# Kernel optimization log

Measured on AMD Instinct MI355X. Metric: run time of the kernel, lower is better.

## Reference

```python
import jax, jax.numpy as jnp
import numpy as np
import math

HEAD = 4
D_MODEL = 128
N_NODES = 2048
SEQ_LEN = 1
D_K = D_MODEL // HEAD
BATCH = 64


def conv1x1_relu(x, w, b):
    # x: [B, C, N, L], w: [O, C], b: [O]  (1x1 Conv2d + ReLU; dropout is identity in eval)
    return jax.nn.relu(jnp.einsum('oc,bcnl->bonl', w, x) + b[None, :, None, None])


def setup_inputs() -> dict:
    key = jax.random.key(0)
    ks = jax.random.split(key, 12)
    s = 0.05
    return {
        'x': jax.random.normal(ks[0], (BATCH, D_MODEL, N_NODES, SEQ_LEN), jnp.float32),
        'q_w': jax.random.normal(ks[1], (D_MODEL, D_MODEL), jnp.float32) * s,
        'q_b': jnp.zeros((D_MODEL,), jnp.float32),
        'v_w': jax.random.normal(ks[2], (D_MODEL, D_MODEL), jnp.float32) * s,
        'v_b': jnp.zeros((D_MODEL,), jnp.float32),
        'c_w': jax.random.normal(ks[3], (D_MODEL, D_MODEL), jnp.float32) * s,
        'c_b': jnp.zeros((D_MODEL,), jnp.float32),
        'memory': jax.random.normal(ks[4], (HEAD, SEQ_LEN, N_NODES, D_K), jnp.float32) * s,
        'nodevec1': jax.random.normal(ks[5], (N_NODES, 10), jnp.float32),
        'nodevec2': jax.random.normal(ks[6], (10, N_NODES), jnp.float32),
        'weights_pool': jax.random.normal(ks[7], (SEQ_LEN, 3, 3), jnp.float32) * s,
        'bias_pool': jax.random.normal(ks[8], (N_NODES, D_K), jnp.float32) * s,
        'aff_w': jnp.ones((D_MODEL, N_NODES, SEQ_LEN), jnp.float32),
        'aff_b': jnp.zeros((D_MODEL, N_NODES, SEQ_LEN), jnp.float32),
    }


def reference(x, q_w, q_b, v_w, v_b, c_w, c_b, memory, nodevec1, nodevec2,
              weights_pool, bias_pool, aff_w, aff_b):
    B = x.shape[0]
    scale = math.sqrt(D_K)

    query = conv1x1_relu(x, q_w, q_b)
    value = conv1x1_relu(x, v_w, v_b)

    # [B, d_model, N, L] -> [B, h, d_k, N, L] -> [B, h, L, N, d_k]
    def split_heads(t):
        return t.reshape(B, HEAD, D_K, N_NODES, SEQ_LEN).transpose(0, 1, 4, 3, 2)

    query = split_heads(query)
    value = split_heads(value)

    key_ = jax.nn.softmax(memory / scale, axis=-1)      # [h, L, N, d_k]
    query = jax.nn.softmax(query / scale, axis=-1)      # [B, h, L, N, d_k]

    Aapt = jax.nn.softmax(jax.nn.relu(nodevec1 @ nodevec2), axis=-1)  # [N, N]

    kv = jnp.einsum('hlnx,bhlny->bhlxy', key_, value)          # [B,h,L,d_k,d_k]
    attn_qkv = jnp.einsum('bhlnx,bhlxy->bhlny', query, kv)     # [B,h,L,N,d_k]

    weights = jnp.einsum('nm,dio->nio', Aapt, weights_pool)    # [N,3,3]
    bias_dyn = Aapt @ bias_pool                                # [N,d_k]
    attn_dyn = jnp.einsum('bhlnc,nio->bhlnc', value, weights) + bias_dyn[None, None, None, :, :]

    out = attn_qkv + attn_dyn                                  # [B,h,L,N,d_k]
    out = out.transpose(0, 1, 4, 3, 2).reshape(B, D_MODEL, N_NODES, SEQ_LEN)
    out = conv1x1_relu(out, c_w, c_b)

    # num_nodes (2048) not in [170, 358, 5] -> affine-residual branch runs
    out = out * aff_w[None] + aff_b[None] + out
    return out
```

## Files before the change

kernel.cpp:

```cpp
#include <hip/hip_runtime.h>

#define NB 64
#define CH 128
#define NNODE 2048
#define NH 4
#define DKK 32
#define INVS 0.17677669529663687f

typedef __bf16 bf16x8 __attribute__((ext_vector_type(8)));
typedef float f32x4 __attribute__((ext_vector_type(4)));
typedef unsigned short ushort_t;

union U16x8 { uint4 u; bf16x8 b; unsigned short s[8]; };

__device__ inline bf16x8 as_bf16x8(uint4 u){ U16x8 x; x.u = u; return x.b; }
__device__ inline unsigned short f2b(float f){ __bf16 h = (__bf16)f; return __builtin_bit_cast(unsigned short, h); }
__device__ inline float b2f(unsigned short u){ __bf16 h = __builtin_bit_cast(__bf16, u); return (float)h; }

__global__ __launch_bounds__(256) void k0_prep(const float* __restrict__ qw,
    const float* __restrict__ vw, const float* __restrict__ cw,
    const float* __restrict__ memory, const float* __restrict__ bias_pool,
    ushort_t* __restrict__ wqb, ushort_t* __restrict__ wvb, ushort_t* __restrict__ wcb,
    ushort_t* __restrict__ keysT, float* __restrict__ bias_dyn,
    ushort_t* __restrict__ bpT)
{
  int gid = blockIdx.x * 256 + threadIdx.x;
  if (gid < 16384) { wqb[gid] = f2b(qw[gid]); wvb[gid] = f2b(vw[gid]); wcb[gid] = f2b(cw[gid]); }
  bias_dyn[gid] = 0.f;
  { int k = gid >> 11, m = gid & 2047;
    bpT[gid] = f2b(bias_pool[m * 32 + k]); }
  if (gid < 8192) {
    int h = gid >> 11, n = gid & 2047;
    const float* src = memory + (size_t)gid * 32;
    float v[32]; float m = -1e30f;
    #pragma unroll
    for (int i = 0; i < 32; ++i) { v[i] = src[i] * INVS; m = fmaxf(m, v[i]); }
    float s = 0.f;
    #pragma unroll
    for (int i = 0; i < 32; ++i) { v[i] = __expf(v[i] - m); s += v[i]; }
    float inv = 1.f / s;
    #pragma unroll
    for (int i = 0; i < 32; ++i)
      keysT[(size_t)(h * 32 + i) * 2048 + n] = f2b(v[i] * inv);
  }
}

__global__ __launch_bounds__(256) void kb1(const float* __restrict__ nv1,
    const float* __restrict__ nv2, ushort_t* __restrict__ Ebuf)
{
  int n = blockIdx.x; int tid = threadIdx.x;
  float a1[10];
  #pragma unroll
  for (int d = 0; d < 10; ++d) a1[d] = nv1[n * 10 + d];
  int m0 = tid * 8;
  float s[8];
  #pragma unroll
  for (int j = 0; j < 8; ++j) s[j] = 0.f;
  #pragma unroll
  for (int d = 0; d < 10; ++d) {
    const float* p = nv2 + d * 2048 + m0;
    float4 u = *(const float4*)p; float4 v = *(const float4*)(p + 4);
    s[0] += a1[d] * u.x; s[1] += a1[d] * u.y; s[2] += a1[d] * u.z; s[3] += a1[d] * u.w;
    s[4] += a1[d] * v.x; s[5] += a1[d] * v.y; s[6] += a1[d] * v.z; s[7] += a1[d] * v.w;
  }
  float e[8]; float sum = 0.f;
  #pragma unroll
  for (int j = 0; j < 8; ++j) { e[j] = __expf(fmaxf(s[j], 0.f)); sum += e[j]; }
  #pragma unroll
  for (int d = 1; d < 64; d <<= 1) sum += __shfl_xor(sum, d);
  __shared__ float red[4];
  if ((tid & 63) == 0) red[tid >> 6] = sum;
  __syncthreads();
  float inv = 1.f / (red[0] + red[1] + red[2] + red[3]);
  U16x8 o;
  #pragma unroll
  for (int j = 0; j < 8; ++j) o.s[j] = f2b(e[j] * inv);
  *(uint4*)(Ebuf + (size_t)n * 2048 + m0) = o.u;
}

__global__ __launch_bounds__(256) void kb2(const ushort_t* __restrict__ Ebuf,
    const ushort_t* __restrict__ bpT, float* __restrict__ bias_dyn)
{
  int bid = blockIdx.x;
  int n0 = (bid >> 3) * 128;
  int m0 = (bid & 7) * 256;
  int tid = threadIdx.x; int wv = tid >> 6; int lane = tid & 63;
  int quad = lane >> 4; int l16 = lane & 15;
  int r0 = n0 + 32 * wv;
  f32x4 zero4 = {0.f,0.f,0.f,0.f};
  f32x4 acc[2][2];
  acc[0][0] = zero4; acc[0][1] = zero4; acc[1][0] = zero4; acc[1][1] = zero4;
  for (int ks = 0; ks < 256; ks += 32) {
    int mb = m0 + ks + 8 * quad;
    bf16x8 a0 = *(const bf16x8*)(Ebuf + (size_t)(r0 + l16) * 2048 + mb);
    bf16x8 a1 = *(const bf16x8*)(Ebuf + (size_t)(r0 + 16 + l16) * 2048 + mb);
    bf16x8 b0 = *(const bf16x8*)(bpT + (size_t)l16 * 2048 + mb);
    bf16x8 b1 = *(const bf16x8*)(bpT + (size_t)(16 + l16) * 2048 + mb);
    acc[0][0] = __builtin_amdgcn_mfma_f32_16x16x32_bf16(a0, b0, acc[0][0], 0, 0, 0);
    acc[0][1] = __builtin_amdgcn_mfma_f32_16x16x32_bf16(a0, b1, acc[0][1], 0, 0, 0);
    acc[1][0] = __builtin_amdgcn_mfma_f32_16x16x32_bf16(a1, b0, acc[1][0], 0, 0, 0);
    acc[1][1] = __builtin_amdgcn_mfma_f32_16x16x32_bf16(a1, b1, acc[1][1], 0, 0, 0);
  }
  #pragma unroll
  for (int rt = 0; rt < 2; ++rt)
    #pragma unroll
    for (int ct = 0; ct < 2; ++ct)
      #pragma unroll
      for (int r = 0; r < 4; ++r)
        atomicAdd(bias_dyn + (size_t)(r0 + 16*rt + 4*quad + r) * 32 + 16*ct + l16,
                  acc[rt][ct][r]);
}

__global__ __launch_bounds__(256) void k1_qv(const float* __restrict__ x,
    const ushort_t* __restrict__ wqb, const ushort_t* __restrict__ wvb,
    const float* __restrict__ qbias, const float* __restrict__ vbias,
    ushort_t* __restrict__ QsT, ushort_t* __restrict__ VT)
{
  int bid = blockIdx.x; int b = bid >> 6; int n0 = (bid & 63) * 32;
  int tid = threadIdx.x; int wv = tid >> 6; int lane = tid & 63;
  int quad = lane >> 4; int l16 = lane & 15;
  __shared__ __align__(16) ushort_t XT[32][136];

  uint4 wq[2][4], wvv[2][4];
  #pragma unroll
  for (int ct = 0; ct < 2; ++ct)
    #pragma unroll
    for (int k0 = 0; k0 < 4; ++k0) {
      int off = (32 * wv + 16 * ct + l16) * 128 + 32 * k0 + 8 * quad;
      wq[ct][k0]  = *(const uint4*)(wqb + off);
      wvv[ct][k0] = *(const uint4*)(wvb + off);
    }
  float qb[2], vb[2];
  #pragma unroll
  for (int ct = 0; ct < 2; ++ct) {
    qb[ct] = qbias[32 * wv + 16 * ct + l16];
    vb[ct] = vbias[32 * wv + 16 * ct + l16];
  }

  #pragma unroll
  for (int p = 0; p < 4; ++p) {
    int c = 32 * p + (tid >> 3); int i = tid & 7;
    float4 v4 = *(const float4*)(x + (size_t)(b * 128 + c) * 2048 + n0 + 4 * i);
    XT[4*i+0][c] = f2b(v4.x); XT[4*i+1][c] = f2b(v4.y);
    XT[4*i+2][c] = f2b(v4.z); XT[4*i+3][c] = f2b(v4.w);
  }
  __syncthreads();

  f32x4 zero4 = {0.f,0.f,0.f,0.f};
  f32x4 accq[2][2], accv[2][2];
  #pragma unroll
  for (int i = 0; i < 2; ++i)
    #pragma unroll
    for (int j = 0; j < 2; ++j) { accq[i][j] = zero4; accv[i][j] = zero4; }

  #pragma unroll
  for (int k0 = 0; k0 < 4; ++k0) {
    bf16x8 a0 = *(const bf16x8*)&XT[l16][32 * k0 + 8 * quad];
    bf16x8 a1 = *(const bf16x8*)&XT[16 + l16][32 * k0 + 8 * quad];
    #pragma unroll
    for (int ct = 0; ct < 2; ++ct) {
      accq[0][ct] = __builtin_amdgcn_mfma_f32_16x16x32_bf16(a0, as_bf16x8(wq[ct][k0]),  accq[0][ct], 0, 0, 0);
      accq[1][ct] = __builtin_amdgcn_mfma_f32_16x16x32_bf16(a1, as_bf16x8(wq[ct][k0]),  accq[1][ct], 0, 0, 0);
      accv[0][ct] = __builtin_amdgcn_mfma_f32_16x16x32_bf16(a0, as_bf16x8(wvv[ct][k0]), accv[0][ct], 0, 0, 0);
      accv[1][ct] = __builtin_amdgcn_mfma_f32_16x16x32_bf16(a1, as_bf16x8(wvv[ct][k0]), accv[1][ct], 0, 0, 0);
    }
  }

  #pragma unroll
  for (int nt = 0; nt < 2; ++nt) {
    float sq[2][4];
    #pragma unroll
    for (int ct = 0; ct < 2; ++ct)
      #pragma unroll
      for (int r = 0; r < 4; ++r)
        sq[ct][r] = fmaxf(accq[nt][ct][r] + qb[ct], 0.f) * INVS;
    #pragma unroll
    for (int r = 0; r < 4; ++r) {
      float m = fmaxf(sq[0][r], sq[1][r]);
      m = fmaxf(m, __shfl_xor(m, 1)); m = fmaxf(m, __shfl_xor(m, 2));
      m = fmaxf(m, __shfl_xor(m, 4)); m = fmaxf(m, __shfl_xor(m, 8));
      float e0 = __expf(sq[0][r] - m), e1 = __expf(sq[1][r] - m);
      float s = e0 + e1;
      s += __shfl_xor(s, 1); s += __shfl_xor(s, 2);
      s += __shfl_xor(s, 4); s += __shfl_xor(s, 8);
      float inv = 1.f / s;
      accq[nt][0][r] = e0 * inv; accq[nt][1][r] = e1 * inv;
    }
    #pragma unroll
    for (int ct = 0; ct < 2; ++ct)
      #pragma unroll
      for (int r = 0; r < 4; ++r)
        accv[nt][ct][r] = fmaxf(accv[nt][ct][r] + vb[ct], 0.f);
  }

  __syncthreads();
  #pragma unroll
  for (int nt = 0; nt < 2; ++nt)
    #pragma unroll
    for (int ct = 0; ct < 2; ++ct)
      #pragma unroll
      for (int r = 0; r < 4; ++r)
        XT[16*nt + 4*quad + r][32*wv + 16*ct + l16] = f2b(accq[nt][ct][r]);
  __syncthreads();
  #pragma unroll
  for (int j = 0; j < 2; ++j) {
    int id = tid + 256 * j; int n = id >> 4; int u = id & 15;
    *(uint4*)(QsT + (size_t)(b * 2048 + n0 + n) * 128 + 8 * u) = *(uint4*)&XT[n][8 * u];
  }
  __syncthreads();
  #pragma unroll
  for (int nt = 0; nt < 2; ++nt)
    #pragma unroll
    for (int ct = 0; ct < 2; ++ct)
      #pragma unroll
      for (int r = 0; r < 4; ++r)
        XT[16*nt + 4*quad + r][32*wv + 16*ct + l16] = f2b(accv[nt][ct][r]);
  __syncthreads();
  #pragma unroll
  for (int j = 0; j < 2; ++j) {
    int id = tid + 256 * j; int n = id >> 4; int u = id & 15;
    *(uint4*)(VT + (size_t)(b * 2048 + n0 + n) * 128 + 8 * u) = *(uint4*)&XT[n][8 * u];
  }
}

__global__ __launch_bounds__(256) void k2_kv(const ushort_t* __restrict__ keysT,
    const ushort_t* __restrict__ VT, float* __restrict__ kvp)
{
  int bid = blockIdx.x; int b = bid >> 3; int nb = (bid & 7) * 256;
  int tid = threadIdx.x; int wv = tid >> 6; int lane = tid & 63;
  int quad = lane >> 4; int l16 = lane & 15;
  __shared__ __align__(16) ushort_t Vraw[128][136];

  f32x4 zero4 = {0.f,0.f,0.f,0.f};
  f32x4 acc[2][2];
  acc[0][0] = zero4; acc[0][1] = zero4; acc[1][0] = zero4; acc[1][1] = zero4;

  for (int chunk = 0; chunk < 2; ++chunk) {
    int nc = nb + 128 * chunk;
    if (chunk) __syncthreads();
    #pragma unroll
    for (int p = 0; p < 8; ++p) {
      int id = tid + 256 * p; int n = id >> 4; int g = id & 15;
      *(uint4*)&Vraw[n][8 * g] = *(const uint4*)(VT + (size_t)(b * 2048 + nc + n) * 128 + 8 * g);
    }
    __syncthreads();
    const ushort_t* kT = keysT + (size_t)(wv * 32) * 2048 + nc;
    #pragma unroll
    for (int ks = 0; ks < 4; ++ks) {
      int k0 = 32 * ks + 8 * quad;
      bf16x8 a0 = *(const bf16x8*)(kT + (size_t)l16 * 2048 + k0);
      bf16x8 a1 = *(const bf16x8*)(kT + (size_t)(16 + l16) * 2048 + k0);
      U16x8 b0, b1;
      #pragma unroll
      for (int j = 0; j < 8; ++j) {
        b0.s[j] = Vraw[k0 + j][32 * wv + l16];
        b1.s[j] = Vraw[k0 + j][32 * wv + 16 + l16];
      }
      acc[0][0] = __builtin_amdgcn_mfma_f32_16x16x32_bf16(a0, b0.b, acc[0][0], 0, 0, 0);
      acc[0][1] = __builtin_amdgcn_mfma_f32_16x16x32_bf16(a0, b1.b, acc[0][1], 0, 0, 0);
      acc[1][0] = __builtin_amdgcn_mfma_f32_16x16x32_bf16(a1, b0.b, acc[1][0], 0, 0, 0);
      acc[1][1] = __builtin_amdgcn_mfma_f32_16x16x32_bf16(a1, b1.b, acc[1][1], 0, 0, 0);
    }
  }

  float* dst = kvp + (size_t)bid * 4096 + wv * 1024;
  #pragma unroll
  for (int yt = 0; yt < 2; ++yt)
    #pragma unroll
    for (int xt = 0; xt < 2; ++xt)
      #pragma unroll
      for (int r = 0; r < 4; ++r)
        dst[(16 * yt + l16) * 32 + 16 * xt + 4 * quad + r] = acc[xt][yt][r];
}

__global__ __launch_bounds__(256) void kred(const float* __restrict__ kvp,
    float* __restrict__ kvws)
{
  int gid = blockIdx.x * 256 + threadIdx.x;
  int b = gid >> 12; int i = gid & 4095;
  const float* p = kvp + (size_t)(b * 8) * 4096 + i;
  float s = 0.f;
  #pragma unroll
  for (int t = 0; t < 8; ++t) s += p[t * 4096];
  kvws[gid] = s;
}

__global__ __launch_bounds__(256) void k3_out(const ushort_t* __restrict__ QsT,
    const ushort_t* __restrict__ VT, const float* __restrict__ kvws,
    const float* __restrict__ bias_dyn, const ushort_t* __restrict__ wcb,
    const float* __restrict__ cbias, const float* __restrict__ wpool,
    const float* __restrict__ aff_w, const float* __restrict__ aff_b,
    float* __restrict__ out)
{
  int bid = blockIdx.x; int b = bid >> 5; int n0 = (bid & 31) * 64;
  int tid = threadIdx.x; int wv = tid >> 6; int lane = tid & 63;
  int quad = lane >> 4; int l16 = lane & 15;
  __shared__ __align__(16) ushort_t kvT[4][32][40];
  __shared__ __align__(16) ushort_t MID[64][136];
  __shared__ __align__(16) ushort_t VL[64][132];
  __shared__ __align__(16) float    BD[64][36];

  float Ws = 0.f;
  #pragma unroll
  for (int i = 0; i < 9; ++i) Ws += wpool[i];

  uint4 wc[2][4];
  #pragma unroll
  for (int mt = 0; mt < 2; ++mt)
    #pragma unroll
    for (int k0 = 0; k0 < 4; ++k0)
      wc[mt][k0] = *(const uint4*)(wcb + (32 * wv + 16 * mt + l16) * 128 + 32 * k0 + 8 * quad);

  #pragma unroll
  for (int p = 0; p < 16; ++p) {
    int id = tid + 256 * p;
    kvT[id >> 10][(id >> 5) & 31][id & 31] = f2b(kvws[(size_t)b * 4096 + id]);
  }
  #pragma unroll
  for (int p = 0; p < 4; ++p) {
    int id = tid + 256 * p; int n = id >> 4; int u = id & 15;
    *(uint4*)&VL[n][8 * u] = *(const uint4*)(VT + (size_t)(b * 2048 + n0 + n) * 128 + 8 * u);
  }
  #pragma unroll
  for (int p = 0; p < 2; ++p) {
    int id = tid + 256 * p; int n = id >> 3; int g = id & 7;
    *(float4*)&BD[n][4 * g] = *(const float4*)(bias_dyn + (size_t)(n0 + n) * 32 + 4 * g);
  }
  __syncthreads();

  f32x4 zero4 = {0.f,0.f,0.f,0.f};
  f32x4 acc1[4][2];
  #pragma unroll
  for (int nt = 0; nt < 4; ++nt) { acc1[nt][0] = zero4; acc1[nt][1] = zero4; }
  #pragma unroll
  for (int nt = 0; nt < 4; ++nt) {
    bf16x8 aq = *(const bf16x8*)(QsT + (size_t)(b * 2048 + n0 + 16 * nt + l16) * 128 + 32 * wv + 8 * quad);
    #pragma unroll
    for (int ct = 0; ct < 2; ++ct)
      acc1[nt][ct] = __builtin_amdgcn_mfma_f32_16x16x32_bf16(
          aq, *(const bf16x8*)&kvT[wv][16 * ct + l16][8 * quad], acc1[nt][ct], 0, 0, 0);
  }

  #pragma unroll
  for (int nt = 0; nt < 4; ++nt)
    #pragma unroll
    for (int ct = 0; ct < 2; ++ct)
      #pragma unroll
      for (int r = 0; r < 4; ++r) {
        int nl = 16 * nt + 4 * quad + r;
        int cc = 32 * wv + 16 * ct + l16;
        float v = b2f(VL[nl][cc]);
        float bd = BD[nl][16 * ct + l16];
        MID[nl][cc] = f2b(acc1[nt][ct][r] + Ws * v + bd);
      }
  __syncthreads();

  f32x4 acc2[2][4];
  #pragma unroll
  for (int mt = 0; mt < 2; ++mt)
    #pragma unroll
    for (int nt = 0; nt < 4; ++nt) acc2[mt][nt] = zero4;
  #pragma unroll
  for (int k0 = 0; k0 < 4; ++k0) {
    bf16x8 bb[4];
    #pragma unroll
    for (int nt = 0; nt < 4; ++nt)
      bb[nt] = *(const bf16x8*)&MID[16 * nt + l16][32 * k0 + 8 * quad];
    #pragma unroll
    for (int mt = 0; mt < 2; ++mt)
      #pragma unroll
      for (int nt = 0; nt < 4; ++nt)
        acc2[mt][nt] = __builtin_amdgcn_mfma_f32_16x16x32_bf16(
            as_bf16x8(wc[mt][k0]), bb[nt], acc2[mt][nt], 0, 0, 0);
  }

  #pragma unroll
  for (int mt = 0; mt < 2; ++mt)
    #pragma unroll
    for (int nt = 0; nt < 4; ++nt)
      #pragma unroll
      for (int r = 0; r < 4; ++r) {
        int c_out = 32 * wv + 16 * mt + 4 * quad + r;
        int nn2 = n0 + 16 * nt + l16;
        float yv = fmaxf(acc2[mt][nt][r] + cbias[c_out], 0.f);
        size_t ai = (size_t)c_out * 2048 + nn2;
        float awv = aff_w[ai], abv = aff_b[ai];
        out[(size_t)(b * 128 + c_out) * 2048 + nn2] = yv * awv + abv + yv;
      }
}

extern "C" void kernel_launch(void* const* d_in, const int* in_sizes, int n_in,
                              void* d_out, int out_size, void* d_ws, size_t ws_size,
                              hipStream_t stream)
{
  const float* x      = (const float*)d_in[0];
  const float* qw     = (const float*)d_in[1];
  const float* qb     = (const float*)d_in[2];
  const float* vw     = (const float*)d_in[3];
  const float* vb     = (const float*)d_in[4];
  const float* cw     = (const float*)d_in[5];
  const float* cb     = (const float*)d_in[6];
  const float* memory = (const float*)d_in[7];
  const float* nv1    = (const float*)d_in[8];
  const float* nv2    = (const float*)d_in[9];
  const float* wpool  = (const float*)d_in[10];
  const float* bpool  = (const float*)d_in[11];
  const float* aw     = (const float*)d_in[12];
  const float* ab     = (const float*)d_in[13];
  float* out = (float*)d_out;

  char* ws = (char*)d_ws;
  ushort_t* QsT      = (ushort_t*)(ws);
  ushort_t* VT       = (ushort_t*)(ws + 33554432);
  float*    kvws     = (float*)   (ws + 67108864);
  ushort_t* keysT    = (ushort_t*)(ws + 68157440);
  float*    bias_dyn = (float*)   (ws + 69206016);
  ushort_t* wqb      = (ushort_t*)(ws + 69468160);
  ushort_t* wvb      = (ushort_t*)(ws + 69500928);
  ushort_t* wcb      = (ushort_t*)(ws + 69533696);
  ushort_t* Ebuf     = (ushort_t*)(ws + 69566464);
  ushort_t* bpT      = (ushort_t*)(ws + 77955072);
  float*    kvp      = (float*)Ebuf;

  k0_prep<<<256, 256, 0, stream>>>(qw, vw, cw, memory, bpool, wqb, wvb, wcb,
                                   keysT, bias_dyn, bpT);
  kb1<<<2048, 256, 0, stream>>>(nv1, nv2, Ebuf);
  kb2<<<128, 256, 0, stream>>>(Ebuf, bpT, bias_dyn);
  k1_qv<<<4096, 256, 0, stream>>>(x, wqb, wvb, qb, vb, QsT, VT);
  k2_kv<<<512, 256, 0, stream>>>(keysT, VT, kvp);
  kred<<<1024, 256, 0, stream>>>(kvp, kvws);
  k3_out<<<2048, 256, 0, stream>>>(QsT, VT, kvws, bias_dyn, wcb, cb, wpool, aw, ab, out);
}
```

Measured before the change: 225.7 us.

## Restructure QV projection kernel with 64-node tiles and transposed MFMA output

The Q/V 1x1-conv kernel now processes 64 nodes per block instead of 32, halving the grid and the number of times each block reloads the weight fragments. The MFMA operands are swapped so each lane holds four consecutive channels, which lets the softmax over d_k reduce with two cross-lane shuffles instead of four and lets results go to shared memory as packed 8-byte stores. The x tile load is reorganised so each thread converts a 4x4 block and writes packed bf16 pairs, cutting scalar LDS stores. A second LDS buffer lets Q and V be staged together and written out in one pass with fewer barriers, at the cost of more shared memory per block and possibly lower occupancy.

```diff
diff --git a/kernel.cpp b/kernel.cpp
--- a/kernel.cpp
+++ b/kernel.cpp
@@ -12,6 +12,7 @@
 typedef unsigned short ushort_t;
 
 union U16x8 { uint4 u; bf16x8 b; unsigned short s[8]; };
+union U16x4 { uint2 u; unsigned short s[4]; };
 
 __device__ inline bf16x8 as_bf16x8(uint4 u){ U16x8 x; x.u = u; return x.b; }
 __device__ inline unsigned short f2b(float f){ __bf16 h = (__bf16)f; return __builtin_bit_cast(unsigned short, h); }
@@ -116,10 +117,11 @@
     const float* __restrict__ qbias, const float* __restrict__ vbias,
     ushort_t* __restrict__ QsT, ushort_t* __restrict__ VT)
 {
-  int bid = blockIdx.x; int b = bid >> 6; int n0 = (bid & 63) * 32;
+  int bid = blockIdx.x; int b = bid >> 5; int n0 = (bid & 31) * 64;
   int tid = threadIdx.x; int wv = tid >> 6; int lane = tid & 63;
   int quad = lane >> 4; int l16 = lane & 15;
-  __shared__ __align__(16) ushort_t XT[32][136];
+  __shared__ __align__(16) ushort_t XT[64][136];
+  __shared__ __align__(16) ushort_t QO[64][136];
 
   uint4 wq[2][4], wvv[2][4];
   #pragma unroll
@@ -130,96 +132,96 @@
       wq[ct][k0]  = *(const uint4*)(wqb + off);
       wvv[ct][k0] = *(const uint4*)(wvb + off);
     }
-  float qb[2], vb[2];
+  float4 qb4[2], vb4[2];
   #pragma unroll
   for (int ct = 0; ct < 2; ++ct) {
-    qb[ct] = qbias[32 * wv + 16 * ct + l16];
-    vb[ct] = vbias[32 * wv + 16 * ct + l16];
-  }
-
-  #pragma unroll
-  for (int p = 0; p < 4; ++p) {
-    int c = 32 * p + (tid >> 3); int i = tid & 7;
-    float4 v4 = *(const float4*)(x + (size_t)(b * 128 + c) * 2048 + n0 + 4 * i);
-    XT[4*i+0][c] = f2b(v4.x); XT[4*i+1][c] = f2b(v4.y);
-    XT[4*i+2][c] = f2b(v4.z); XT[4*i+3][c] = f2b(v4.w);
+    qb4[ct] = *(const float4*)(qbias + 32 * wv + 16 * ct + 4 * quad);
+    vb4[ct] = *(const float4*)(vbias + 32 * wv + 16 * ct + 4 * quad);
+  }
+
+  #pragma unroll
+  for (int p = 0; p < 2; ++p) {
+    int c4 = 4 * ((tid >> 4) + 16 * p);
+    int n4 = 4 * (tid & 15);
+    float4 r[4];
+    #pragma unroll
+    for (int j = 0; j < 4; ++j)
+      r[j] = *(const float4*)(x + (size_t)(b * 128 + c4 + j) * 2048 + n0 + n4);
+    #pragma unroll
+    for (int i = 0; i < 4; ++i) {
+      U16x4 w;
+      w.s[0] = f2b(((const float*)&r[0])[i]);
+      w.s[1] = f2b(((const float*)&r[1])[i]);
+      w.s[2] = f2b(((const float*)&r[2])[i]);
+      w.s[3] = f2b(((const float*)&r[3])[i]);
+      *(uint2*)&XT[n4 + i][c4] = w.u;
+    }
   }
   __syncthreads();
 
   f32x4 zero4 = {0.f,0.f,0.f,0.f};
-  f32x4 accq[2][2], accv[2][2];
-  #pragma unroll
-  for (int i = 0; i < 2; ++i)
-    #pragma unroll
-    for (int j = 0; j < 2; ++j) { accq[i][j] = zero4; accv[i][j] = zero4; }
-
-  #pragma unroll
-  for (int k0 = 0; k0 < 4; ++k0) {
-    bf16x8 a0 = *(const bf16x8*)&XT[l16][32 * k0 + 8 * quad];
-    bf16x8 a1 = *(const bf16x8*)&XT[16 + l16][32 * k0 + 8 * quad];
+  f32x4 av[4][2];
+
+  #pragma unroll
+  for (int nt = 0; nt < 4; ++nt) {
+    f32x4 aq[2]; aq[0] = zero4; aq[1] = zero4;
+    f32x4 avv[2]; avv[0] = zero4; avv[1] = zero4;
+    #pragma unroll
+    for (int k0 = 0; k0 < 4; ++k0) {
+      bf16x8 bfrag = *(const bf16x8*)&XT[16 * nt + l16][32 * k0 + 8 * quad];
+      #pragma unroll
+      for (int ct = 0; ct < 2; ++ct) {
+        aq[ct]  = __builtin_amdgcn_mfma_f32_16x16x32_bf16(as_bf16x8(wq[ct][k0]),  bfrag, aq[ct],  0, 0, 0);
+        avv[ct] = __builtin_amdgcn_mfma_f32_16x16x32_bf16(as_bf16x8(wvv[ct][k0]), bfrag, avv[ct], 0, 0, 0);
+      }
+    }
+    float sq[2][4]; float mx = -1e30f;
+    #pragma unroll
+    for (int ct = 0; ct < 2; ++ct)
+      #pragma unroll
+      for (int r = 0; r < 4; ++r) {
+        sq[ct][r] = fmaxf(aq[ct][r] + ((const float*)&qb4[ct])[r], 0.f) * INVS;
+        mx = fmaxf(mx, sq[ct][r]);
+      }
+    mx = fmaxf(mx, __shfl_xor(mx, 16));
+    mx = fmaxf(mx, __shfl_xor(mx, 32));
+    float sum = 0.f;
+    #pragma unroll
+    for (int ct = 0; ct < 2; ++ct)
+      #pragma unroll
+      for (int r = 0; r < 4; ++r) { sq[ct][r] = __expf(sq[ct][r] - mx); sum += sq[ct][r]; }
+    sum += __shfl_xor(sum, 16);
+    sum += __shfl_xor(sum, 32);
+    float inv = 1.f / sum;
     #pragma unroll
     for (int ct = 0; ct < 2; ++ct) {
-      accq[0][ct] = __builtin_amdgcn_mfma_f32_16x16x32_bf16(a0, as_bf16x8(wq[ct][k0]),  accq[0][ct], 0, 0, 0);
-      accq[1][ct] = __builtin_amdgcn_mfma_f32_16x16x32_bf16(a1, as_bf16x8(wq[ct][k0]),  accq[1][ct], 0, 0, 0);
-      accv[0][ct] = __builtin_amdgcn_mfma_f32_16x16x32_bf16(a0, as_bf16x8(wvv[ct][k0]), accv[0][ct], 0, 0, 0);
-      accv[1][ct] = __builtin_amdgcn_mfma_f32_16x16x32_bf16(a1, as_bf16x8(wvv[ct][k0]), accv[1][ct], 0, 0, 0);
-    }
-  }
-
-  #pragma unroll
-  for (int nt = 0; nt < 2; ++nt) {
-    float sq[2][4];
-    #pragma unroll
-    for (int ct = 0; ct < 2; ++ct)
+      U16x4 w;
+      #pragma unroll
+      for (int r = 0; r < 4; ++r) w.s[r] = f2b(sq[ct][r] * inv);
+      *(uint2*)&QO[16 * nt + l16][32 * wv + 16 * ct + 4 * quad] = w.u;
+    }
+    av[nt][0] = avv[0]; av[nt][1] = avv[1];
+  }
+  __syncthreads();
+
+  #pragma unroll
+  for (int nt = 0; nt < 4; ++nt)
+    #pragma unroll
+    for (int ct = 0; ct < 2; ++ct) {
+      U16x4 w;
       #pragma unroll
       for (int r = 0; r < 4; ++r)
-        sq[ct][r] = fmaxf(accq[nt][ct][r] + qb[ct], 0.f) * INVS;
-    #pragma unroll
-    for (int r = 0; r < 4; ++r) {
-      float m = fmaxf(sq[0][r], sq[1][r]);
-      m = fmaxf(m, __shfl_xor(m, 1)); m = fmaxf(m, __shfl_xor(m, 2));
-      m = fmaxf(m, __shfl_xor(m, 4)); m = fmaxf(m, __shfl_xor(m, 8));
-      float e0 = __expf(sq[0][r] - m), e1 = __expf(sq[1][r] - m);
-      float s = e0 + e1;
-      s += __shfl_xor(s, 1); s += __shfl_xor(s, 2);
-      s += __shfl_xor(s, 4); s += __shfl_xor(s, 8);
-      float inv = 1.f / s;
-      accq[nt][0][r] = e0 * inv; accq[nt][1][r] = e1 * inv;
-    }
-    #pragma unroll
-    for (int ct = 0; ct < 2; ++ct)
-      #pragma unroll
-      for (int r = 0; r < 4; ++r)
-        accv[nt][ct][r] = fmaxf(accv[nt][ct][r] + vb[ct], 0.f);
-  }
-
-  __syncthreads();
-  #pragma unroll
-  for (int nt = 0; nt < 2; ++nt)
-    #pragma unroll
-    for (int ct = 0; ct < 2; ++ct)
-      #pragma unroll
-      for (int r = 0; r < 4; ++r)
-        XT[16*nt + 4*quad + r][32*wv + 16*ct + l16] = f2b(accq[nt][ct][r]);
-  __syncthreads();
-  #pragma unroll
-  for (int j = 0; j < 2; ++j) {
+        w.s[r] = f2b(fmaxf(av[nt][ct][r] + ((const float*)&vb4[ct])[r], 0.f));
+      *(uint2*)&XT[16 * nt + l16][32 * wv + 16 * ct + 4 * quad] = w.u;
+    }
+  __syncthreads();
+
+  #pragma unroll
+  for (int j = 0; j < 4; ++j) {
     int id = tid + 256 * j; int n = id >> 4; int u = id & 15;
-    *(uint4*)(QsT + (size_t)(b * 2048 + n0 + n) * 128 + 8 * u) = *(uint4*)&XT[n][8 * u];
-  }
-  __syncthreads();
-  #pragma unroll
-  for (int nt = 0; nt < 2; ++nt)
-    #pragma unroll
-    for (int ct = 0; ct < 2; ++ct)
-      #pragma unroll
-      for (int r = 0; r < 4; ++r)
-        XT[16*nt + 4*quad + r][32*wv + 16*ct + l16] = f2b(accv[nt][ct][r]);
-  __syncthreads();
-  #pragma unroll
-  for (int j = 0; j < 2; ++j) {
-    int id = tid + 256 * j; int n = id >> 4; int u = id & 15;
-    *(uint4*)(VT + (size_t)(b * 2048 + n0 + n) * 128 + 8 * u) = *(uint4*)&XT[n][8 * u];
+    size_t go = (size_t)(b * 2048 + n0 + n) * 128 + 8 * u;
+    *(uint4*)(QsT + go) = *(uint4*)&QO[n][8 * u];
+    *(uint4*)(VT  + go) = *(uint4*)&XT[n][8 * u];
   }
 }
 
@@ -426,7 +428,7 @@
                                    keysT, bias_dyn, bpT);
   kb1<<<2048, 256, 0, stream>>>(nv1, nv2, Ebuf);
   kb2<<<128, 256, 0, stream>>>(Ebuf, bpT, bias_dyn);
-  k1_qv<<<4096, 256, 0, stream>>>(x, wqb, wvb, qb, vb, QsT, VT);
+  k1_qv<<<2048, 256, 0, stream>>>(x, wqb, wvb, qb, vb, QsT, VT);
   k2_kv<<<512, 256, 0, stream>>>(keysT, VT, kvp);
   kred<<<1024, 256, 0, stream>>>(kvp, kvws);
   k3_out<<<2048, 256, 0, stream>>>(QsT, VT, kvws, bias_dyn, wcb, cb, wpool, aw, ab, out);
```

After: 212.6 us. -5.8%, faster.
